# Optimization experiments

Measured on AMD Instinct MI355X. Metric: run time of the kernel, lower is better.

Reference implementation:

```python
import jax, jax.numpy as jnp
import numpy as np

N, T, D, P, NB = 32768, 128, 32, 16, 15


def setup_inputs() -> dict:
    key = jax.random.key(0)
    ks = jax.random.split(key, 8)
    S = jax.random.normal(ks[0], (N, T, 1), dtype=jnp.float32)
    L_dyn = jax.random.normal(ks[1], (N, T, D), dtype=jnp.float32)
    C_static = jax.random.normal(ks[2], (N, P), dtype=jnp.float32)
    Y = jax.random.randint(ks[3], (N, T, 1), 0, 2).astype(jnp.float32)
    mask = jnp.ones((N, T), dtype=jnp.float32)
    return {
        "S": S, "L_dyn": L_dyn, "C_static": C_static, "Y": Y, "mask": mask,
        "psi": jnp.array([0.5], jnp.float32),
        "gamma_A": jnp.array([0.1], jnp.float32),
        "w_gamma_dyn": 0.05 * jax.random.normal(ks[4], (D,), dtype=jnp.float32),
        "w_gamma_static": 0.05 * jax.random.normal(ks[5], (P,), dtype=jnp.float32),
        "log_sigma_Z": jnp.array([-0.5], jnp.float32),
        "beta_0": jnp.array([-4.0], jnp.float32),
        "beta_Z": jnp.array([0.3], jnp.float32),
        "beta_bins": jnp.zeros((NB,), jnp.float32),
        "w_beta_dyn": 0.1 * jax.random.normal(ks[6], (D,), dtype=jnp.float32),
        "w_beta_static": 0.1 * jax.random.normal(ks[7], (P,), dtype=jnp.float32),
        "beta_time": jnp.array([0.03], jnp.float32),
    }


def reference(S, L_dyn, C_static, Y, mask, psi, gamma_A, w_gamma_dyn,
              w_gamma_static, log_sigma_Z, beta_0, beta_Z, beta_bins,
              w_beta_dyn, w_beta_static, beta_time):
    n, t_len = S.shape[0], S.shape[1]
    nb = beta_bins.shape[0]
    edges = jnp.linspace(-2.5, 2.5, nb + 1).astype(S.dtype)
    # torch.bucketize(s, edges[1:-1]) (right=False) == searchsorted side='left'
    idx = jnp.clip(jnp.searchsorted(edges[1:-1], S[..., 0], side='left'), 0, nb - 1)
    bin_eff = beta_bins[idx][..., None]            # (N,T,1) == (A_bin * beta_bins).sum(-1)
    sigma_sq = jnp.exp(log_sigma_Z)[0] ** 2        # sigma_Z^2
    gd = L_dyn @ w_gamma_dyn[:, None]              # (N,T,1) gamma_dyn(L)
    bd = L_dyn @ w_beta_dyn[:, None]               # (N,T,1) beta_dyn(L)
    gs = (C_static @ w_gamma_static)[:, None]      # (N,1) gamma_static(C)
    bs = (C_static @ w_beta_static)[:, None]       # (N,1) beta_static(C)
    tt = jnp.arange(t_len, dtype=S.dtype) / 30.0   # beta_time * (t/30)

    xs = (
        jnp.swapaxes(S, 0, 1),        # (T,N,1)
        jnp.swapaxes(gd, 0, 1),
        jnp.swapaxes(bd, 0, 1),
        jnp.swapaxes(bin_eff, 0, 1),
        jnp.swapaxes(Y, 0, 1),
        mask.T[:, :, None],           # (T,N,1)
        tt,
    )
    psi_s, gA, bZ, b0, bT = psi[0], gamma_A[0], beta_Z[0], beta_0[0], beta_time[0]

    def step(carry, x):
        Z_mean, Z_var, ll = carry
        A_t, gd_t, bd_t, be_t, Y_t, m_t, t_s = x
        # latent transition prior
        Z_pred_mean = psi_s * Z_mean + gA * A_t + gd_t + gs
        Z_pred_var = psi_s ** 2 * Z_var + sigma_sq
        # outcome probability
        logit = b0 + bZ * Z_pred_mean + be_t + bd_t + bs + bT * t_s
        prob = jax.nn.sigmoid(jnp.clip(logit, -20.0, 20.0))
        # approximate Kalman (Laplace) update from Y
        grad = (Y_t - prob) * bZ * m_t
        hess = bZ ** 2 * prob * (1.0 - prob) * m_t + 1e-6
        Z_post_var = 1.0 / (1.0 / (Z_pred_var + 1e-8) + hess)
        Z_post_mean = Z_pred_mean + Z_post_var * grad
        ll_t = ((Y_t * jnp.log(prob + 1e-10)
                 + (1.0 - Y_t) * jnp.log(1.0 - prob + 1e-10)) * m_t).sum()
        return (Z_post_mean, Z_post_var, ll + ll_t), (Z_post_mean, Z_post_var)

    init = (jnp.zeros((n, 1), S.dtype), jnp.ones((n, 1), S.dtype),
            jnp.zeros((), S.dtype))
    (_, _, ll), (Zf, Zv) = jax.lax.scan(step, init, xs)
    return jnp.swapaxes(Zf, 0, 1), jnp.swapaxes(Zv, 0, 1), ll
```

## Files before the change

kernel.cpp:

```cpp
#include <hip/hip_runtime.h>

#define T_LEN 128
#define NB_BINS 15

__global__ __launch_bounds__(256) void k_fused(
    const float4* __restrict__ S4,
    const float4* __restrict__ Y4,
    const float4* __restrict__ M4,
    const float4* __restrict__ C4,
    const float4* __restrict__ L4,
    const float4* __restrict__ wgd4,
    const float4* __restrict__ wbd4,
    const float4* __restrict__ wgs4,
    const float4* __restrict__ wbs4,
    const float*  __restrict__ p_psi,
    const float*  __restrict__ p_gA,
    const float*  __restrict__ p_lsz,
    const float*  __restrict__ p_b0,
    const float*  __restrict__ p_bZ,
    const float*  __restrict__ p_bbins,
    const float*  __restrict__ p_bT,
    float* __restrict__ zf,
    float* __restrict__ zv,
    float* __restrict__ ll_out)
{
    __shared__ float sbins[NB_BINS];
    if (threadIdx.x < NB_BINS) sbins[threadIdx.x] = p_bbins[threadIdx.x];
    __syncthreads();

    const int gtid = blockIdx.x * blockDim.x + threadIdx.x;
    const int n = gtid >> 2;
    const int s = gtid & 3;

    const float4 wga = wgd4[s],     wgb = wgd4[s + 4];
    const float4 wba = wbd4[s],     wbb = wbd4[s + 4];

    const float psi  = p_psi[0];
    const float gA   = p_gA[0];
    const float e    = __expf(p_lsz[0]);
    const float sig2 = e * e;
    const float b0   = p_b0[0];
    const float bZ   = p_bZ[0];
    const float bT30 = p_bT[0] * (1.0f / 30.0f);
    const float psi2 = psi * psi;
    const float bZ2  = bZ * bZ;

    float gs, bs;
    {
        const float4 c  = C4[n * 4 + s];
        const float4 wg = wgs4[s];
        const float4 wb = wbs4[s];
        gs = c.x * wg.x + c.y * wg.y + c.z * wg.z + c.w * wg.w;
        bs = c.x * wb.x + c.y * wb.y + c.z * wb.z + c.w * wb.w;
        gs += __shfl_xor(gs, 1, 64); gs += __shfl_xor(gs, 2, 64);
        bs += __shfl_xor(bs, 1, 64); bs += __shfl_xor(bs, 2, 64);
    }

    const size_t lb  = (size_t)n * T_LEN * 8;
    const int    sbi = n * (T_LEN / 4);

    float4 Lc0 = L4[lb + 0*8 + s], Lc1 = L4[lb + 0*8 + 4 + s];
    float4 Lc2 = L4[lb + 1*8 + s], Lc3 = L4[lb + 1*8 + 4 + s];
    float4 Lc4 = L4[lb + 2*8 + s], Lc5 = L4[lb + 2*8 + 4 + s];
    float4 Lc6 = L4[lb + 3*8 + s], Lc7 = L4[lb + 3*8 + 4 + s];
    float4 sc = S4[sbi], yc = Y4[sbi], mc = M4[sbi];

    float zm = 0.0f, zvv = 1.0f, ll = 0.0f;

#define STEP(J, LA, LB, SS, YY, MM, PMOUT, PVOUT, PROBOUT) do {               \
        const float s_v = (SS), y_v = (YY), m_v = (MM);                       \
        float g   = LA.x*wga.x + LA.y*wga.y + LA.z*wga.z + LA.w*wga.w         \
                  + LB.x*wgb.x + LB.y*wgb.y + LB.z*wgb.z + LB.w*wgb.w;        \
        float bdv = LA.x*wba.x + LA.y*wba.y + LA.z*wba.z + LA.w*wba.w         \
                  + LB.x*wbb.x + LB.y*wbb.y + LB.z*wbb.z + LB.w*wbb.w;        \
        g   += __shfl_xor(g,   1, 64); g   += __shfl_xor(g,   2, 64);         \
        bdv += __shfl_xor(bdv, 1, 64); bdv += __shfl_xor(bdv, 2, 64);         \
        int cnt = (int)fmaxf(0.0f, fminf(14.0f,                               \
                      ceilf(fmaf(s_v, 3.0f, 7.5f)) - 1.0f));                  \
        const float be    = sbins[cnt];                                       \
        const float zpm   = psi * zm + gA * s_v + g + gs;                     \
        const float zpv   = psi2 * zvv + sig2;                                \
        float logit = b0 + bZ * zpm + be + bdv + bs                           \
                    + bT30 * (float)(4 * k + (J));                            \
        logit = fminf(fmaxf(logit, -20.0f), 20.0f);                           \
        const float prob  = __builtin_amdgcn_rcpf(1.0f + __expf(-logit));     \
        const float grad  = (y_v - prob) * bZ * m_v;                          \
        const float hess  = bZ2 * prob * (1.0f - prob) * m_v + 1e-6f;         \
        const float pvv   = __builtin_amdgcn_rcpf(                            \
                   __builtin_amdgcn_rcpf(zpv + 1e-8f) + hess);                \
        const float pmm   = zpm + pvv * grad;                                 \
        zm = pmm; zvv = pvv; PMOUT = pmm; PVOUT = pvv; PROBOUT = prob;        \
    } while (0)

    for (int k = 0; k < T_LEN / 4; ++k) {
        const int kn = (k + 1 < T_LEN / 4) ? (k + 1) : k;
        const size_t lbn = lb + (size_t)(4 * kn) * 8;
        float4 Ln0 = L4[lbn + 0*8 + s], Ln1 = L4[lbn + 0*8 + 4 + s];
        float4 Ln2 = L4[lbn + 1*8 + s], Ln3 = L4[lbn + 1*8 + 4 + s];
        float4 Ln4 = L4[lbn + 2*8 + s], Ln5 = L4[lbn + 2*8 + 4 + s];
        float4 Ln6 = L4[lbn + 3*8 + s], Ln7 = L4[lbn + 3*8 + 4 + s];
        float4 snn = S4[sbi + kn], ynn = Y4[sbi + kn], mnn = M4[sbi + kn];

        float pm0, pm1, pm2, pm3, pv0, pv1, pv2, pv3, pr0, pr1, pr2, pr3;
        STEP(0, Lc0, Lc1, sc.x, yc.x, mc.x, pm0, pv0, pr0);
        STEP(1, Lc2, Lc3, sc.y, yc.y, mc.y, pm1, pv1, pr1);
        STEP(2, Lc4, Lc5, sc.z, yc.z, mc.z, pm2, pv2, pr2);
        STEP(3, Lc6, Lc7, sc.w, yc.w, mc.w, pm3, pv3, pr3);

        const float pmsel = (s == 0) ? pm0 : (s == 1) ? pm1 : (s == 2) ? pm2 : pm3;
        const float pvsel = (s == 0) ? pv0 : (s == 1) ? pv1 : (s == 2) ? pv2 : pv3;
        const size_t oidx = (size_t)n * T_LEN + 4 * k + s;
        zf[oidx] = pmsel;
        zv[oidx] = pvsel;

        {
            const float prs = (s == 0) ? pr0 : (s == 1) ? pr1 : (s == 2) ? pr2 : pr3;
            const float ys  = (s == 0) ? yc.x : (s == 1) ? yc.y : (s == 2) ? yc.z : yc.w;
            const float ms  = (s == 0) ? mc.x : (s == 1) ? mc.y : (s == 2) ? mc.z : mc.w;
            ll += (ys * __logf(prs + 1e-10f)
                 + (1.0f - ys) * __logf(1.0f - prs + 1e-10f)) * ms;
        }

        Lc0 = Ln0; Lc1 = Ln1; Lc2 = Ln2; Lc3 = Ln3;
        Lc4 = Ln4; Lc5 = Ln5; Lc6 = Ln6; Lc7 = Ln7;
        sc = snn; yc = ynn; mc = mnn;
    }
#undef STEP

    #pragma unroll
    for (int off = 1; off < 64; off <<= 1) ll += __shfl_xor(ll, off, 64);
    if ((threadIdx.x & 63) == 0) atomicAdd(ll_out, ll);
}

extern "C" void kernel_launch(void* const* d_in, const int* in_sizes, int n_in,
                              void* d_out, int out_size, void* d_ws, size_t ws_size,
                              hipStream_t stream) {
    const float* S     = (const float*)d_in[0];
    const float* L     = (const float*)d_in[1];
    const float* C     = (const float*)d_in[2];
    const float* Y     = (const float*)d_in[3];
    const float* M     = (const float*)d_in[4];
    const float* psi   = (const float*)d_in[5];
    const float* gA    = (const float*)d_in[6];
    const float* wgd   = (const float*)d_in[7];
    const float* wgs   = (const float*)d_in[8];
    const float* lsz   = (const float*)d_in[9];
    const float* b0    = (const float*)d_in[10];
    const float* bZ    = (const float*)d_in[11];
    const float* bbins = (const float*)d_in[12];
    const float* wbd   = (const float*)d_in[13];
    const float* wbs   = (const float*)d_in[14];
    const float* bT    = (const float*)d_in[15];

    const int NT    = in_sizes[0];
    const int n_seq = NT / T_LEN;

    float* zf = (float*)d_out;
    float* zv = zf + NT;
    float* ll = zf + 2 * (size_t)NT;

    hipMemsetAsync((void*)ll, 0, sizeof(float), stream);

    const int threads = 256;
    const int blocks  = (n_seq * 4) / threads;
    k_fused<<<blocks, threads, 0, stream>>>(
        reinterpret_cast<const float4*>(S),
        reinterpret_cast<const float4*>(Y),
        reinterpret_cast<const float4*>(M),
        reinterpret_cast<const float4*>(C),
        reinterpret_cast<const float4*>(L),
        reinterpret_cast<const float4*>(wgd),
        reinterpret_cast<const float4*>(wbd),
        reinterpret_cast<const float4*>(wgs),
        reinterpret_cast<const float4*>(wbs),
        psi, gA, lsz, b0, bZ, bbins, bT,
        zf, zv, ll);
}
```

Baseline: 173.1 us.

## Split fused scan into static, parallel precompute, and lean recurrence kernels

The single fused kernel is split into three. A static-projection kernel computes gs/bs per sequence. A grid-stride precompute kernel does the L_dyn dot products, bin lookup and time term for every (n,t) row and writes them into the output buffers. A scan kernel then runs only the sequential Kalman recurrence on those precomputed values, storing results as float4. The aim is to take the bandwidth-heavy L reads and the shuffle reductions off the serial dependency chain. In exchange the intermediates make an extra write and read round trip through memory, and there are more kernel launches.

Measured after the change: 182.2 us. +5.3%, slower.

```diff
diff --git a/kernel.cpp b/kernel.cpp
--- a/kernel.cpp
+++ b/kernel.cpp
@@ -3,128 +3,185 @@
 #define T_LEN 128
 #define NB_BINS 15
 
-__global__ __launch_bounds__(256) void k_fused(
-    const float4* __restrict__ S4,
-    const float4* __restrict__ Y4,
-    const float4* __restrict__ M4,
+__global__ __launch_bounds__(256) void k_static(
     const float4* __restrict__ C4,
+    const float4* __restrict__ wgs4,
+    const float4* __restrict__ wbs4,
+    float* __restrict__ gs_out, float* __restrict__ bs_out, int n_seq)
+{
+    int n = blockIdx.x * blockDim.x + threadIdx.x;
+    if (n >= n_seq) return;
+    float gs = 0.0f, bs = 0.0f;
+    #pragma unroll
+    for (int i = 0; i < 4; ++i) {
+        float4 c = C4[n * 4 + i];
+        float4 wg = wgs4[i];
+        float4 wb = wbs4[i];
+        gs += c.x * wg.x + c.y * wg.y + c.z * wg.z + c.w * wg.w;
+        bs += c.x * wb.x + c.y * wb.y + c.z * wb.z + c.w * wb.w;
+    }
+    gs_out[n] = gs;
+    bs_out[n] = bs;
+}
+
+__global__ __launch_bounds__(256) void k_pre(
     const float4* __restrict__ L4,
+    const float*  __restrict__ S,
+    const float*  __restrict__ gs_in,
+    const float*  __restrict__ bs_in,
     const float4* __restrict__ wgd4,
     const float4* __restrict__ wbd4,
-    const float4* __restrict__ wgs4,
-    const float4* __restrict__ wbs4,
-    const float*  __restrict__ p_psi,
     const float*  __restrict__ p_gA,
-    const float*  __restrict__ p_lsz,
     const float*  __restrict__ p_b0,
-    const float*  __restrict__ p_bZ,
     const float*  __restrict__ p_bbins,
     const float*  __restrict__ p_bT,
-    float* __restrict__ zf,
-    float* __restrict__ zv,
-    float* __restrict__ ll_out)
+    float* __restrict__ a_out,
+    float* __restrict__ c_out,
+    int total_rows)
 {
     __shared__ float sbins[NB_BINS];
     if (threadIdx.x < NB_BINS) sbins[threadIdx.x] = p_bbins[threadIdx.x];
     __syncthreads();
 
+    const float gA   = p_gA[0];
+    const float b0   = p_b0[0];
+    const float bT30 = p_bT[0] * (1.0f / 30.0f);
+
+    const int tid   = blockIdx.x * blockDim.x + threadIdx.x;
+    const int lane8 = tid & 7;
+    const float4 wg = wgd4[lane8];
+    const float4 wb = wbd4[lane8];
+
+    const int group   = tid >> 3;
+    const int ngroups = (gridDim.x * blockDim.x) >> 3;
+
+    int row = group;
+    float4 v = (row < total_rows) ? L4[(size_t)row * 8 + lane8]
+                                  : make_float4(0, 0, 0, 0);
+    for (; row < total_rows; row += ngroups) {
+        const int nrow = row + ngroups;
+        float4 vn = v;
+        if (nrow < total_rows) vn = L4[(size_t)nrow * 8 + lane8];
+
+        float g = v.x * wg.x + v.y * wg.y + v.z * wg.z + v.w * wg.w;
+        float b = v.x * wb.x + v.y * wb.y + v.z * wb.z + v.w * wb.w;
+        #pragma unroll
+        for (int off = 1; off < 8; off <<= 1) {
+            g += __shfl_xor(g, off, 64);
+            b += __shfl_xor(b, off, 64);
+        }
+
+        const int n = row >> 7;
+        const int t = row & 127;
+        const float s_v = S[row];
+        const float gsv = gs_in[n];
+        const float bsv = bs_in[n];
+        int cnt = (int)fmaxf(0.0f, fminf(14.0f,
+                      ceilf(fmaf(s_v, 3.0f, 7.5f)) - 1.0f));
+        const float a = gA * s_v + g + gsv;
+        const float c = b0 + sbins[cnt] + b + bsv + bT30 * (float)t;
+
+        if (lane8 == 0) { a_out[row] = a; c_out[row] = c; }
+        v = vn;
+    }
+}
+
+__global__ __launch_bounds__(256) void k_scan(
+    const float4* Ain,
+    const float4* Cin,
+    const float4* __restrict__ Y4,
+    const float4* __restrict__ M4,
+    const float*  __restrict__ p_psi,
+    const float*  __restrict__ p_lsz,
+    const float*  __restrict__ p_bZ,
+    float4* Zf4,
+    float4* Zv4,
+    float* __restrict__ ll_out)
+{
     const int gtid = blockIdx.x * blockDim.x + threadIdx.x;
     const int n = gtid >> 2;
     const int s = gtid & 3;
 
-    const float4 wga = wgd4[s],     wgb = wgd4[s + 4];
-    const float4 wba = wbd4[s],     wbb = wbd4[s + 4];
-
     const float psi  = p_psi[0];
-    const float gA   = p_gA[0];
     const float e    = __expf(p_lsz[0]);
     const float sig2 = e * e;
-    const float b0   = p_b0[0];
     const float bZ   = p_bZ[0];
-    const float bT30 = p_bT[0] * (1.0f / 30.0f);
     const float psi2 = psi * psi;
     const float bZ2  = bZ * bZ;
 
-    float gs, bs;
-    {
-        const float4 c  = C4[n * 4 + s];
-        const float4 wg = wgs4[s];
-        const float4 wb = wbs4[s];
-        gs = c.x * wg.x + c.y * wg.y + c.z * wg.z + c.w * wg.w;
-        bs = c.x * wb.x + c.y * wb.y + c.z * wb.z + c.w * wb.w;
-        gs += __shfl_xor(gs, 1, 64); gs += __shfl_xor(gs, 2, 64);
-        bs += __shfl_xor(bs, 1, 64); bs += __shfl_xor(bs, 2, 64);
+    const int b32 = n * 32;
+
+    float zm = 0.0f, zvv = 1.0f, ll = 0.0f;
+
+#define STEP(AA, CC, YY, MM, PMOUT, PVOUT, PROUT) do {                    \
+        const float zpm = fmaf(psi, zm, (AA));                            \
+        const float zpv = fmaf(psi2, zvv, sig2);                          \
+        float logit = fmaf(bZ, zpm, (CC));                                \
+        logit = fminf(fmaxf(logit, -20.0f), 20.0f);                       \
+        const float prob = __builtin_amdgcn_rcpf(1.0f + __expf(-logit));  \
+        const float grad = ((YY) - prob) * bZ * (MM);                     \
+        const float hess = fmaf(bZ2 * prob * (1.0f - prob), (MM), 1e-6f); \
+        const float pvv  = __builtin_amdgcn_rcpf(                         \
+                             __builtin_amdgcn_rcpf(zpv + 1e-8f) + hess);  \
+        const float pmm  = fmaf(pvv, grad, zpm);                          \
+        zm = pmm; zvv = pvv;                                              \
+        PMOUT = pmm; PVOUT = pvv; PROUT = prob;                           \
+    } while (0)
+
+#define CHUNK(J, Aq, Cq, Yq, Mq) do {                                     \
+        float pm0, pm1, pm2, pm3, pv0, pv1, pv2, pv3, pr0, pr1, pr2, pr3; \
+        STEP(Aq.x, Cq.x, Yq.x, Mq.x, pm0, pv0, pr0);                      \
+        STEP(Aq.y, Cq.y, Yq.y, Mq.y, pm1, pv1, pr1);                      \
+        STEP(Aq.z, Cq.z, Yq.z, Mq.z, pm2, pv2, pr2);                      \
+        STEP(Aq.w, Cq.w, Yq.w, Mq.w, pm3, pv3, pr3);                      \
+        const float prs = (s == 0) ? pr0 : (s == 1) ? pr1                 \
+                        : (s == 2) ? pr2 : pr3;                           \
+        const float ys  = (s == 0) ? Yq.x : (s == 1) ? Yq.y               \
+                        : (s == 2) ? Yq.z : Yq.w;                         \
+        const float ms  = (s == 0) ? Mq.x : (s == 1) ? Mq.y               \
+                        : (s == 2) ? Mq.z : Mq.w;                         \
+        ll += (ys * __logf(prs + 1e-10f)                                  \
+             + (1.0f - ys) * __logf(1.0f - prs + 1e-10f)) * ms;           \
+        if (s == (J)) {                                                   \
+            stpm = make_float4(pm0, pm1, pm2, pm3);                       \
+            stpv = make_float4(pv0, pv1, pv2, pv3);                       \
+        }                                                                 \
+    } while (0)
+
+    float4 A0 = Ain[b32 + 0], A1 = Ain[b32 + 1], A2 = Ain[b32 + 2], A3 = Ain[b32 + 3];
+    float4 C0 = Cin[b32 + 0], C1 = Cin[b32 + 1], C2 = Cin[b32 + 2], C3 = Cin[b32 + 3];
+    float4 Y0 = Y4[b32 + 0],  Y1 = Y4[b32 + 1],  Y2 = Y4[b32 + 2],  Y3 = Y4[b32 + 3];
+    float4 M0 = M4[b32 + 0],  M1 = M4[b32 + 1],  M2 = M4[b32 + 2],  M3 = M4[b32 + 3];
+
+    for (int Q = 0; Q < 8; ++Q) {
+        float4 An0, An1, An2, An3, Cn0, Cn1, Cn2, Cn3;
+        float4 Yn0, Yn1, Yn2, Yn3, Mn0, Mn1, Mn2, Mn3;
+        if (Q < 7) {
+            const int qb = b32 + 4 * (Q + 1);
+            An0 = Ain[qb + 0]; An1 = Ain[qb + 1]; An2 = Ain[qb + 2]; An3 = Ain[qb + 3];
+            Cn0 = Cin[qb + 0]; Cn1 = Cin[qb + 1]; Cn2 = Cin[qb + 2]; Cn3 = Cin[qb + 3];
+            Yn0 = Y4[qb + 0];  Yn1 = Y4[qb + 1];  Yn2 = Y4[qb + 2];  Yn3 = Y4[qb + 3];
+            Mn0 = M4[qb + 0];  Mn1 = M4[qb + 1];  Mn2 = M4[qb + 2];  Mn3 = M4[qb + 3];
+        }
+
+        float4 stpm = make_float4(0, 0, 0, 0);
+        float4 stpv = make_float4(0, 0, 0, 0);
+        CHUNK(0, A0, C0, Y0, M0);
+        CHUNK(1, A1, C1, Y1, M1);
+        CHUNK(2, A2, C2, Y2, M2);
+        CHUNK(3, A3, C3, Y3, M3);
+
+        Zf4[b32 + 4 * Q + s] = stpm;
+        Zv4[b32 + 4 * Q + s] = stpv;
+
+        if (Q < 7) {
+            A0 = An0; A1 = An1; A2 = An2; A3 = An3;
+            C0 = Cn0; C1 = Cn1; C2 = Cn2; C3 = Cn3;
+            Y0 = Yn0; Y1 = Yn1; Y2 = Yn2; Y3 = Yn3;
+            M0 = Mn0; M1 = Mn1; M2 = Mn2; M3 = Mn3;
+        }
     }
-
-    const size_t lb  = (size_t)n * T_LEN * 8;
-    const int    sbi = n * (T_LEN / 4);
-
-    float4 Lc0 = L4[lb + 0*8 + s], Lc1 = L4[lb + 0*8 + 4 + s];
-    float4 Lc2 = L4[lb + 1*8 + s], Lc3 = L4[lb + 1*8 + 4 + s];
-    float4 Lc4 = L4[lb + 2*8 + s], Lc5 = L4[lb + 2*8 + 4 + s];
-    float4 Lc6 = L4[lb + 3*8 + s], Lc7 = L4[lb + 3*8 + 4 + s];
-    float4 sc = S4[sbi], yc = Y4[sbi], mc = M4[sbi];
-
-    float zm = 0.0f, zvv = 1.0f, ll = 0.0f;
-
-#define STEP(J, LA, LB, SS, YY, MM, PMOUT, PVOUT, PROBOUT) do {               \
-        const float s_v = (SS), y_v = (YY), m_v = (MM);                       \
-        float g   = LA.x*wga.x + LA.y*wga.y + LA.z*wga.z + LA.w*wga.w         \
-                  + LB.x*wgb.x + LB.y*wgb.y + LB.z*wgb.z + LB.w*wgb.w;        \
-        float bdv = LA.x*wba.x + LA.y*wba.y + LA.z*wba.z + LA.w*wba.w         \
-                  + LB.x*wbb.x + LB.y*wbb.y + LB.z*wbb.z + LB.w*wbb.w;        \
-        g   += __shfl_xor(g,   1, 64); g   += __shfl_xor(g,   2, 64);         \
-        bdv += __shfl_xor(bdv, 1, 64); bdv += __shfl_xor(bdv, 2, 64);         \
-        int cnt = (int)fmaxf(0.0f, fminf(14.0f,                               \
-                      ceilf(fmaf(s_v, 3.0f, 7.5f)) - 1.0f));                  \
-        const float be    = sbins[cnt];                                       \
-        const float zpm   = psi * zm + gA * s_v + g + gs;                     \
-        const float zpv   = psi2 * zvv + sig2;                                \
-        float logit = b0 + bZ * zpm + be + bdv + bs                           \
-                    + bT30 * (float)(4 * k + (J));                            \
-        logit = fminf(fmaxf(logit, -20.0f), 20.0f);                           \
-        const float prob  = __builtin_amdgcn_rcpf(1.0f + __expf(-logit));     \
-        const float grad  = (y_v - prob) * bZ * m_v;                          \
-        const float hess  = bZ2 * prob * (1.0f - prob) * m_v + 1e-6f;         \
-        const float pvv   = __builtin_amdgcn_rcpf(                            \
-                   __builtin_amdgcn_rcpf(zpv + 1e-8f) + hess);                \
-        const float pmm   = zpm + pvv * grad;                                 \
-        zm = pmm; zvv = pvv; PMOUT = pmm; PVOUT = pvv; PROBOUT = prob;        \
-    } while (0)
-
-    for (int k = 0; k < T_LEN / 4; ++k) {
-        const int kn = (k + 1 < T_LEN / 4) ? (k + 1) : k;
-        const size_t lbn = lb + (size_t)(4 * kn) * 8;
-        float4 Ln0 = L4[lbn + 0*8 + s], Ln1 = L4[lbn + 0*8 + 4 + s];
-        float4 Ln2 = L4[lbn + 1*8 + s], Ln3 = L4[lbn + 1*8 + 4 + s];
-        float4 Ln4 = L4[lbn + 2*8 + s], Ln5 = L4[lbn + 2*8 + 4 + s];
-        float4 Ln6 = L4[lbn + 3*8 + s], Ln7 = L4[lbn + 3*8 + 4 + s];
-        float4 snn = S4[sbi + kn], ynn = Y4[sbi + kn], mnn = M4[sbi + kn];
-
-        float pm0, pm1, pm2, pm3, pv0, pv1, pv2, pv3, pr0, pr1, pr2, pr3;
-        STEP(0, Lc0, Lc1, sc.x, yc.x, mc.x, pm0, pv0, pr0);
-        STEP(1, Lc2, Lc3, sc.y, yc.y, mc.y, pm1, pv1, pr1);
-        STEP(2, Lc4, Lc5, sc.z, yc.z, mc.z, pm2, pv2, pr2);
-        STEP(3, Lc6, Lc7, sc.w, yc.w, mc.w, pm3, pv3, pr3);
-
-        const float pmsel = (s == 0) ? pm0 : (s == 1) ? pm1 : (s == 2) ? pm2 : pm3;
-        const float pvsel = (s == 0) ? pv0 : (s == 1) ? pv1 : (s == 2) ? pv2 : pv3;
-        const size_t oidx = (size_t)n * T_LEN + 4 * k + s;
-        zf[oidx] = pmsel;
-        zv[oidx] = pvsel;
-
-        {
-            const float prs = (s == 0) ? pr0 : (s == 1) ? pr1 : (s == 2) ? pr2 : pr3;
-            const float ys  = (s == 0) ? yc.x : (s == 1) ? yc.y : (s == 2) ? yc.z : yc.w;
-            const float ms  = (s == 0) ? mc.x : (s == 1) ? mc.y : (s == 2) ? mc.z : mc.w;
-            ll += (ys * __logf(prs + 1e-10f)
-                 + (1.0f - ys) * __logf(1.0f - prs + 1e-10f)) * ms;
-        }
-
-        Lc0 = Ln0; Lc1 = Ln1; Lc2 = Ln2; Lc3 = Ln3;
-        Lc4 = Ln4; Lc5 = Ln5; Lc6 = Ln6; Lc7 = Ln7;
-        sc = snn; yc = ynn; mc = mnn;
-    }
+#undef CHUNK
 #undef STEP
 
     #pragma unroll
@@ -159,20 +216,32 @@
     float* zv = zf + NT;
     float* ll = zf + 2 * (size_t)NT;
 
+    float* gs_ws = (float*)d_ws;
+    float* bs_ws = gs_ws + n_seq;
+
     hipMemsetAsync((void*)ll, 0, sizeof(float), stream);
 
-    const int threads = 256;
-    const int blocks  = (n_seq * 4) / threads;
-    k_fused<<<blocks, threads, 0, stream>>>(
-        reinterpret_cast<const float4*>(S),
+    k_static<<<(n_seq + 255) / 256, 256, 0, stream>>>(
+        reinterpret_cast<const float4*>(C),
+        reinterpret_cast<const float4*>(wgs),
+        reinterpret_cast<const float4*>(wbs),
+        gs_ws, bs_ws, n_seq);
+
+    k_pre<<<2048, 256, 0, stream>>>(
+        reinterpret_cast<const float4*>(L),
+        S, gs_ws, bs_ws,
+        reinterpret_cast<const float4*>(wgd),
+        reinterpret_cast<const float4*>(wbd),
+        gA, b0, bbins, bT,
+        zf, zv, NT);
+
+    k_scan<<<(n_seq * 4) / 256, 256, 0, stream>>>(
+        reinterpret_cast<const float4*>(zf),
+        reinterpret_cast<const float4*>(zv),
         reinterpret_cast<const float4*>(Y),
         reinterpret_cast<const float4*>(M),
-        reinterpret_cast<const float4*>(C),
-        reinterpret_cast<const float4*>(L),
-        reinterpret_cast<const float4*>(wgd),
-        reinterpret_cast<const float4*>(wbd),
-        reinterpret_cast<const float4*>(wgs),
-        reinterpret_cast<const float4*>(wbs),
-        psi, gA, lsz, b0, bZ, bbins, bT,
-        zf, zv, ll);
-}
+        psi, lsz, bZ,
+        reinterpret_cast<float4*>(zf),
+        reinterpret_cast<float4*>(zv),
+        ll);
+}
```

## Split each sequence across eight lanes with triple-buffered prefetch and nontemporal stores

Applied to the files above, without the earlier changes.

Each sequence is now handled by 8 lanes instead of 4, so each lane loads a single float4 of L per timestep and the dot-product reduction gains a third shuffle. Loads are software-pipelined two chunks ahead with three rotating register buffers. Outputs are written by one owner lane per pair of timesteps using nontemporal stores. The aim is more memory-level parallelism and twice as many waves to hide the bandwidth-bound L read, at the cost of duplicated recurrence work per lane and extra shuffles.

Result: faster. 168.9 us, median of 2 (-2.4%).

```diff
diff --git a/kernel.cpp b/kernel.cpp
--- a/kernel.cpp
+++ b/kernel.cpp
@@ -3,7 +3,7 @@
 #define T_LEN 128
 #define NB_BINS 15
 
-__global__ __launch_bounds__(256) void k_fused(
+__global__ __launch_bounds__(256, 4) void k_fused8(
     const float4* __restrict__ S4,
     const float4* __restrict__ Y4,
     const float4* __restrict__ M4,
@@ -22,18 +22,18 @@
     const float*  __restrict__ p_bT,
     float* __restrict__ zf,
     float* __restrict__ zv,
-    float* __restrict__ ll_out)
+    float*  __restrict__ ll_out)
 {
     __shared__ float sbins[NB_BINS];
     if (threadIdx.x < NB_BINS) sbins[threadIdx.x] = p_bbins[threadIdx.x];
     __syncthreads();
 
     const int gtid = blockIdx.x * blockDim.x + threadIdx.x;
-    const int n = gtid >> 2;
-    const int s = gtid & 3;
+    const int n = gtid >> 3;
+    const int j = gtid & 7;
 
-    const float4 wga = wgd4[s],     wgb = wgd4[s + 4];
-    const float4 wba = wbd4[s],     wbb = wbd4[s + 4];
+    const float4 wg = wgd4[j];
+    const float4 wb = wbd4[j];
 
     const float psi  = p_psi[0];
     const float gA   = p_gA[0];
@@ -47,85 +47,92 @@
 
     float gs, bs;
     {
-        const float4 c  = C4[n * 4 + s];
-        const float4 wg = wgs4[s];
-        const float4 wb = wbs4[s];
-        gs = c.x * wg.x + c.y * wg.y + c.z * wg.z + c.w * wg.w;
-        bs = c.x * wb.x + c.y * wb.y + c.z * wb.z + c.w * wb.w;
+        const float4 c  = C4[n * 4 + (j & 3)];
+        const float4 wgsv = wgs4[j & 3];
+        const float4 wbsv = wbs4[j & 3];
+        gs = c.x * wgsv.x + c.y * wgsv.y + c.z * wgsv.z + c.w * wgsv.w;
+        bs = c.x * wbsv.x + c.y * wbsv.y + c.z * wbsv.z + c.w * wbsv.w;
         gs += __shfl_xor(gs, 1, 64); gs += __shfl_xor(gs, 2, 64);
         bs += __shfl_xor(bs, 1, 64); bs += __shfl_xor(bs, 2, 64);
     }
 
-    const size_t lb  = (size_t)n * T_LEN * 8;
-    const int    sbi = n * (T_LEN / 4);
-
-    float4 Lc0 = L4[lb + 0*8 + s], Lc1 = L4[lb + 0*8 + 4 + s];
-    float4 Lc2 = L4[lb + 1*8 + s], Lc3 = L4[lb + 1*8 + 4 + s];
-    float4 Lc4 = L4[lb + 2*8 + s], Lc5 = L4[lb + 2*8 + 4 + s];
-    float4 Lc6 = L4[lb + 3*8 + s], Lc7 = L4[lb + 3*8 + 4 + s];
-    float4 sc = S4[sbi], yc = Y4[sbi], mc = M4[sbi];
+    const size_t lb = (size_t)n * 1024;
+    const int    sb = n * 32;
 
     float zm = 0.0f, zvv = 1.0f, ll = 0.0f;
+    float pmS0 = 0.f, pmS1 = 0.f, pvS0 = 0.f, pvS1 = 0.f;
 
-#define STEP(J, LA, LB, SS, YY, MM, PMOUT, PVOUT, PROBOUT) do {               \
+#define LOAD(P, c) do {                                                       \
+        const size_t rb = lb + (size_t)(c) * 32 + j;                          \
+        P##0 = L4[rb];      P##1 = L4[rb + 8];                                \
+        P##2 = L4[rb + 16]; P##3 = L4[rb + 24];                               \
+        P##s = S4[sb + (c)]; P##y = Y4[sb + (c)]; P##m = M4[sb + (c)];        \
+    } while (0)
+
+#define STEP(i, Lv, SS, YY, MM, c) do {                                       \
         const float s_v = (SS), y_v = (YY), m_v = (MM);                       \
-        float g   = LA.x*wga.x + LA.y*wga.y + LA.z*wga.z + LA.w*wga.w         \
-                  + LB.x*wgb.x + LB.y*wgb.y + LB.z*wgb.z + LB.w*wgb.w;        \
-        float bdv = LA.x*wba.x + LA.y*wba.y + LA.z*wba.z + LA.w*wba.w         \
-                  + LB.x*wbb.x + LB.y*wbb.y + LB.z*wbb.z + LB.w*wbb.w;        \
+        float g   = Lv.x*wg.x + Lv.y*wg.y + Lv.z*wg.z + Lv.w*wg.w;            \
+        float bdv = Lv.x*wb.x + Lv.y*wb.y + Lv.z*wb.z + Lv.w*wb.w;            \
         g   += __shfl_xor(g,   1, 64); g   += __shfl_xor(g,   2, 64);         \
+        g   += __shfl_xor(g,   4, 64);                                        \
         bdv += __shfl_xor(bdv, 1, 64); bdv += __shfl_xor(bdv, 2, 64);         \
+        bdv += __shfl_xor(bdv, 4, 64);                                        \
         int cnt = (int)fmaxf(0.0f, fminf(14.0f,                               \
                       ceilf(fmaf(s_v, 3.0f, 7.5f)) - 1.0f));                  \
-        const float be    = sbins[cnt];                                       \
-        const float zpm   = psi * zm + gA * s_v + g + gs;                     \
-        const float zpv   = psi2 * zvv + sig2;                                \
+        const float be   = sbins[cnt];                                        \
+        const float zpm  = psi * zm + gA * s_v + g + gs;                      \
+        const float zpv  = psi2 * zvv + sig2;                                 \
         float logit = b0 + bZ * zpm + be + bdv + bs                           \
-                    + bT30 * (float)(4 * k + (J));                            \
+                    + bT30 * (float)(4 * (c) + (i));                          \
         logit = fminf(fmaxf(logit, -20.0f), 20.0f);                           \
-        const float prob  = __builtin_amdgcn_rcpf(1.0f + __expf(-logit));     \
-        const float grad  = (y_v - prob) * bZ * m_v;                          \
-        const float hess  = bZ2 * prob * (1.0f - prob) * m_v + 1e-6f;         \
-        const float pvv   = __builtin_amdgcn_rcpf(                            \
+        const float prob = __builtin_amdgcn_rcpf(1.0f + __expf(-logit));      \
+        const float grad = (y_v - prob) * bZ * m_v;                           \
+        const float hess = bZ2 * prob * (1.0f - prob) * m_v + 1e-6f;          \
+        const float pvv  = __builtin_amdgcn_rcpf(                             \
                    __builtin_amdgcn_rcpf(zpv + 1e-8f) + hess);                \
-        const float pmm   = zpm + pvv * grad;                                 \
-        zm = pmm; zvv = pvv; PMOUT = pmm; PVOUT = pvv; PROBOUT = prob;        \
+        const float pmm  = zpm + pvv * grad;                                  \
+        zm = pmm; zvv = pvv;                                                  \
+           \
+        if (j == (((c) & 3) * 2 + ((i) >> 1))) {                              \
+            if ((i) & 1) { pmS1 = pmm; pvS1 = pvv; }                          \
+            else         { pmS0 = pmm; pvS0 = pvv; }                          \
+            ll += (y_v * __logf(prob + 1e-10f)                                \
+                 + (1.0f - y_v) * __logf(1.0f - prob + 1e-10f)) * m_v;        \
+        }                                                                     \
     } while (0)
 
-    for (int k = 0; k < T_LEN / 4; ++k) {
-        const int kn = (k + 1 < T_LEN / 4) ? (k + 1) : k;
-        const size_t lbn = lb + (size_t)(4 * kn) * 8;
-        float4 Ln0 = L4[lbn + 0*8 + s], Ln1 = L4[lbn + 0*8 + 4 + s];
-        float4 Ln2 = L4[lbn + 1*8 + s], Ln3 = L4[lbn + 1*8 + 4 + s];
-        float4 Ln4 = L4[lbn + 2*8 + s], Ln5 = L4[lbn + 2*8 + 4 + s];
-        float4 Ln6 = L4[lbn + 3*8 + s], Ln7 = L4[lbn + 3*8 + 4 + s];
-        float4 snn = S4[sbi + kn], ynn = Y4[sbi + kn], mnn = M4[sbi + kn];
+#define COMP(P, c) do {                                                       \
+        STEP(0, P##0, P##s.x, P##y.x, P##m.x, c);                             \
+        STEP(1, P##1, P##s.y, P##y.y, P##m.y, c);                             \
+        STEP(2, P##2, P##s.z, P##y.z, P##m.z, c);                             \
+        STEP(3, P##3, P##s.w, P##y.w, P##m.w, c);                             \
+        if (((c) & 3) == 3) {        \
+            const size_t ob = (size_t)n * 128 + ((c) >> 2) * 16 + j * 2;      \
+            __builtin_nontemporal_store(pmS0, &zf[ob]);                       \
+            __builtin_nontemporal_store(pmS1, &zf[ob + 1]);                   \
+            __builtin_nontemporal_store(pvS0, &zv[ob]);                       \
+            __builtin_nontemporal_store(pvS1, &zv[ob + 1]);                   \
+        }                                                                     \
+    } while (0)
 
-        float pm0, pm1, pm2, pm3, pv0, pv1, pv2, pv3, pr0, pr1, pr2, pr3;
-        STEP(0, Lc0, Lc1, sc.x, yc.x, mc.x, pm0, pv0, pr0);
-        STEP(1, Lc2, Lc3, sc.y, yc.y, mc.y, pm1, pv1, pr1);
-        STEP(2, Lc4, Lc5, sc.z, yc.z, mc.z, pm2, pv2, pr2);
-        STEP(3, Lc6, Lc7, sc.w, yc.w, mc.w, pm3, pv3, pr3);
+    float4 A0, A1, A2, A3, As, Ay, Am;
+    float4 B0, B1, B2, B3, Bs, By, Bm;
+    float4 D0, D1, D2, D3, Ds, Dy, Dm;
 
-        const float pmsel = (s == 0) ? pm0 : (s == 1) ? pm1 : (s == 2) ? pm2 : pm3;
-        const float pvsel = (s == 0) ? pv0 : (s == 1) ? pv1 : (s == 2) ? pv2 : pv3;
-        const size_t oidx = (size_t)n * T_LEN + 4 * k + s;
-        zf[oidx] = pmsel;
-        zv[oidx] = pvsel;
+    LOAD(A, 0);
+    LOAD(B, 1);
 
-        {
-            const float prs = (s == 0) ? pr0 : (s == 1) ? pr1 : (s == 2) ? pr2 : pr3;
-            const float ys  = (s == 0) ? yc.x : (s == 1) ? yc.y : (s == 2) ? yc.z : yc.w;
-            const float ms  = (s == 0) ? mc.x : (s == 1) ? mc.y : (s == 2) ? mc.z : mc.w;
-            ll += (ys * __logf(prs + 1e-10f)
-                 + (1.0f - ys) * __logf(1.0f - prs + 1e-10f)) * ms;
-        }
+    for (int k = 0; k < 30; k += 3) {
+        LOAD(D, k + 2); COMP(A, k);
+        LOAD(A, k + 3); COMP(B, k + 1);
+        LOAD(B, k + 4); COMP(D, k + 2);
+    }
+    COMP(A, 30);
+    COMP(B, 31);
 
-        Lc0 = Ln0; Lc1 = Ln1; Lc2 = Ln2; Lc3 = Ln3;
-        Lc4 = Ln4; Lc5 = Ln5; Lc6 = Ln6; Lc7 = Ln7;
-        sc = snn; yc = ynn; mc = mnn;
-    }
+#undef COMP
 #undef STEP
+#undef LOAD
 
     #pragma unroll
     for (int off = 1; off < 64; off <<= 1) ll += __shfl_xor(ll, off, 64);
@@ -162,8 +169,8 @@
     hipMemsetAsync((void*)ll, 0, sizeof(float), stream);
 
     const int threads = 256;
-    const int blocks  = (n_seq * 4) / threads;
-    k_fused<<<blocks, threads, 0, stream>>>(
+    const int blocks  = (n_seq * 8) / threads;
+    k_fused8<<<blocks, threads, 0, stream>>>(
         reinterpret_cast<const float4*>(S),
         reinterpret_cast<const float4*>(Y),
         reinterpret_cast<const float4*>(M),
```
